# Optimization experiments

Measured on AMD Instinct MI355X. Metric: run time of the kernel, lower is better.

## Reference

```python
import jax, jax.numpy as jnp
import numpy as np

LAYERS, STACKS, K = 10, 3, 2
DILATIONS = [2 ** i for _ in range(STACKS) for i in range(LAYERS)]  # 30 layers


def conv1d(x, w, b=None, dilation=1):
    # x: [N, C_in, T], w: [C_out, C_in, K] (torch Conv1d layout), VALID padding
    out = jax.lax.conv_general_dilated(
        x, w, window_strides=(1,), padding='VALID',
        rhs_dilation=(dilation,), dimension_numbers=('NCH', 'OIH', 'NCH'))
    if b is not None:
        out = out + b[None, :, None]
    return out


def setup_inputs() -> dict:
    key = jax.random.key(0)
    ks = jax.random.split(key, 12)
    s = 0.1  # weight scale to avoid gate saturation
    return {
        'y': jax.random.normal(ks[0], (16, 1, 16384), dtype=jnp.float32),
        'causal_w': jax.random.normal(ks[1], (32, 1, 1), dtype=jnp.float32) * s,
        'causal_b': jax.random.normal(ks[2], (32,), dtype=jnp.float32) * s,
        'filt_w': jax.random.normal(ks[3], (30, 32, 32, K), dtype=jnp.float32) * s,
        'gate_w': jax.random.normal(ks[4], (30, 32, 32, K), dtype=jnp.float32) * s,
        'res_w': jax.random.normal(ks[5], (30, 32, 32, 1), dtype=jnp.float32) * s,
        'skip_w': jax.random.normal(ks[6], (30, 256, 32, 1), dtype=jnp.float32) * s,
        'end1_w': jax.random.normal(ks[7], (256, 256, 1), dtype=jnp.float32) * s,
        'end1_b': jax.random.normal(ks[8], (256,), dtype=jnp.float32) * s,
        'end2_w': jax.random.normal(ks[9], (256, 256, 1), dtype=jnp.float32) * s,
        'end2_b': jax.random.normal(ks[10], (256,), dtype=jnp.float32) * s,
    }


def reference(y, causal_w, causal_b, filt_w, gate_w, res_w, skip_w,
              end1_w, end1_b, end2_w, end2_b):
    x = conv1d(y, causal_w, causal_b)  # [B, 32, T]
    skip = None
    for i, d in enumerate(DILATIONS):
        r = x
        f = jnp.tanh(conv1d(x, filt_w[i], dilation=d))      # [B,32,T-d]
        g = jax.nn.sigmoid(conv1d(x, gate_w[i], dilation=d))
        x = f * g
        s = conv1d(x, skip_w[i])                             # [B,256,T-d]
        t = s.shape[-1]
        skip = s if skip is None else s + skip[:, :, -t:]
        x = conv1d(x, res_w[i])
        x = x + r[:, :, -x.shape[-1]:]
    x = jax.nn.relu(skip)
    x = jax.nn.relu(conv1d(x, end1_w, end1_b))
    x = conv1d(x, end2_w, end2_b)
    return x
```

## Files before the change

### kernel.cpp

```cpp
#include <hip/hip_runtime.h>
#include <hip/hip_bf16.h>
#include <cstdint>

#define NB 16
#define NC 32
#define T0 16384
#define NL 30
#define SKC 256
#define TF 13315
#define WGRP 192
#define XBC 320
#define XBS 20

typedef _Float16 f16;
typedef _Float16 f16x2 __attribute__((ext_vector_type(2)));
typedef _Float16 f16x8 __attribute__((ext_vector_type(8)));
typedef float f32x4 __attribute__((ext_vector_type(4)));
typedef uint32_t u32;

#define MFMA16(a,b,c) __builtin_amdgcn_mfma_f32_16x16x32_f16(a,b,c,0,0,0)

#define SCF (-2.88539008f)
#define SCG (-1.44269504f)
#define CLF 86.6f
#define CLG 43.3f

__device__ __forceinline__ float frcp(float x){
#if __has_builtin(__builtin_amdgcn_rcpf)
  return __builtin_amdgcn_rcpf(x);
#else
  return 1.f/x;
#endif
}
__device__ __forceinline__ float fexp2(float x){
#if __has_builtin(__builtin_amdgcn_exp2f)
  return __builtin_amdgcn_exp2f(x);
#else
  return exp2f(x);
#endif
}
__device__ __forceinline__ float clampf(float x, float c){
#if __has_builtin(__builtin_amdgcn_fmed3f)
  return __builtin_amdgcn_fmed3f(x, -c, c);
#else
  return fminf(fmaxf(x, -c), c);
#endif
}
__device__ __forceinline__ u32 pk2(float x, float y){
#if __has_builtin(__builtin_amdgcn_cvt_pkrtz)
  return __builtin_bit_cast(u32, __builtin_amdgcn_cvt_pkrtz(x, y));
#else
  f16x2 r; r.x = (f16)x; r.y = (f16)y;
  return __builtin_bit_cast(u32, r);
#endif
}
__device__ __forceinline__ u32 pkadd(u32 a, u32 b){
  f16x2 s = __builtin_bit_cast(f16x2, a) + __builtin_bit_cast(f16x2, b);
  return __builtin_bit_cast(u32, s);
}
#if __has_builtin(__builtin_amdgcn_global_load_lds)
#define HAVE_GLL 1
__device__ __forceinline__ void gll16(const void* g, void* l){
  __builtin_amdgcn_global_load_lds(
      (const __attribute__((address_space(1))) u32*)g,
      (__attribute__((address_space(3))) u32*)l, 16, 0, 0);
}
#else
#define HAVE_GLL 0
#endif
__device__ __forceinline__ size_t zfrag_off(int lz, int q){
  return (size_t)(lz & ~63)*NC + (size_t)(((lz>>4)&3)*512 + (q*16 + (lz&15))*8);
}
__device__ __forceinline__ int sigma_co(int q, int j){
  return (j < 4) ? (4*q + j) : (12 + 4*q + j);
}

__global__ __launch_bounds__(256) void prep3(
    const float* __restrict__ sw, const float* __restrict__ e1w,
    const float* __restrict__ e2w, const float* __restrict__ fw,
    const float* __restrict__ gw, const float* __restrict__ rw,
    f16* __restrict__ wsk, f16* __restrict__ e1f, f16* __restrict__ e2f,
    f16* __restrict__ fgpf, f16* __restrict__ ggpf, u32* __restrict__ rwp){
  int idx = blockIdx.x*256 + threadIdx.x;
  if (idx < 30720){
    int lane = idx & 63, mt = (idx>>6)&15, i = idx>>10;
    int m = mt*16 + (lane&15);
    int q = lane >> 4;
    const float* s = sw + ((size_t)i*SKC + m)*NC;
    f16* dp = wsk + (size_t)idx*8;
    #pragma unroll
    for (int j=0;j<8;j++) dp[j] = (f16)s[sigma_co(q, j)];
  } else if (idx < 38912){
    int j2 = idx - 30720;
    int lane = j2&63, mt = (j2>>6)&15, ks = j2>>10;
    int m = mt*16 + (lane&15);
    int k = ks*32 + (lane>>4)*8;
    const float* s = e1w + (size_t)m*SKC + k;
    f16* dp = e1f + (size_t)j2*8;
    #pragma unroll
    for (int j=0;j<8;j++) dp[j] = (f16)s[j];
  } else if (idx < 47104){
    int j2 = idx - 38912;
    int lane = j2&63, mt = (j2>>6)&15, ks = j2>>10;
    int m = mt*16 + (lane&15);
    int k = ks*32 + (lane>>4)*8;
    const float* s = e2w + (size_t)m*SKC + k;
    f16* dp = e2f + (size_t)j2*8;
    #pragma unroll
    for (int j=0;j<8;j++) dp[j] = (f16)s[j];
  } else if (idx < 77824){
    int j2 = idx - 47104;
    const float* s = fw + (size_t)j2*2;
    size_t base = (size_t)(j2 >> 5) * 64;
    int ci = j2 & 31;
    fgpf[base + ci]      = (f16)(s[0]*SCF);
    fgpf[base + 32 + ci] = (f16)(s[1]*SCF);
  } else if (idx < 108544){
    int j2 = idx - 77824;
    const float* s = gw + (size_t)j2*2;
    size_t base = (size_t)(j2 >> 5) * 64;
    int ci = j2 & 31;
    ggpf[base + ci]      = (f16)(s[0]*SCG);
    ggpf[base + 32 + ci] = (f16)(s[1]*SCG);
  } else if (idx < 123904){
    int j2 = idx - 108544;
    int i = j2 >> 9, c = (j2>>4)&31, pj = j2&15;
    const float* s = rw + ((size_t)i*NC + c)*NC;
    int q = pj >> 2, j0 = (2*pj) & 7;
    int c0 = sigma_co(q, j0);
    f16x2 p; p.x = (f16)s[c0]; p.y = (f16)s[c0+1];
    rwp[j2] = __builtin_bit_cast(u32, p);
  }
}

struct LW { f16x8 af[4]; f16x8 ag[4]; f16x8 ar[2]; };
__device__ __forceinline__ void lw_load(LW& w, const f16* __restrict__ fp,
    const f16* __restrict__ gp, const u32* __restrict__ rp, int lane){
  int m = lane & 15, q8 = (lane >> 4) * 8, q4 = (lane >> 4) * 4;
  #pragma unroll
  for (int mh = 0; mh < 2; mh++){
    #pragma unroll
    for (int tap = 0; tap < 2; tap++){
      w.af[mh*2+tap] = *(const f16x8*)&fp[((mh*16+m)*2+tap)*32 + q8];
      w.ag[mh*2+tap] = *(const f16x8*)&gp[((mh*16+m)*2+tap)*32 + q8];
    }
    w.ar[mh] = *(const f16x8*)&rp[(mh*16+m)*16 + q4];
  }
}

__device__ __forceinline__ void tile_core(const LW& w,
    uint4 a, uint4 b, uint2 rb0, uint2 rb1,
    uint4& zfrag, uint2& xo0, uint2& xo1){
  f16x8 A  = __builtin_bit_cast(f16x8, a);
  f16x8 Bt = __builtin_bit_cast(f16x8, b);
  f32x4 z4 = {0.f,0.f,0.f,0.f};
  f32x4 fa0 = MFMA16(w.af[0], A, z4); fa0 = MFMA16(w.af[1], Bt, fa0);
  f32x4 fa1 = MFMA16(w.af[2], A, z4); fa1 = MFMA16(w.af[3], Bt, fa1);
  f32x4 ga0 = MFMA16(w.ag[0], A, z4); ga0 = MFMA16(w.ag[1], Bt, ga0);
  f32x4 ga1 = MFMA16(w.ag[2], A, z4); ga1 = MFMA16(w.ag[3], Bt, ga1);
  u32 zq[4];
  #pragma unroll
  for (int mh = 0; mh < 2; mh++){
    f32x4 fv = mh ? fa1 : fa0;
    f32x4 gv = mh ? ga1 : ga0;
    float zz[4];
    #pragma unroll
    for (int r = 0; r < 4; r++){
      float t = fexp2(clampf(fv[r], CLF));
      float u = fexp2(clampf(gv[r], CLG));
      zz[r] = (1.f - t) * frcp((1.f + t) * (1.f + u));
    }
    zq[mh*2+0] = pk2(zz[0], zz[1]);
    zq[mh*2+1] = pk2(zz[2], zz[3]);
  }
  zfrag = make_uint4(zq[0], zq[1], zq[2], zq[3]);
  f16x8 zB = __builtin_bit_cast(f16x8, zfrag);
  f32x4 r0 = MFMA16(w.ar[0], zB, z4);
  f32x4 r1 = MFMA16(w.ar[1], zB, z4);
  xo0.x = pkadd(pk2(r0[0], r0[1]), rb0.x);
  xo0.y = pkadd(pk2(r0[2], r0[3]), rb0.y);
  xo1.x = pkadd(pk2(r1[0], r1[1]), rb1.x);
  xo1.y = pkadd(pk2(r1[2], r1[3]), rb1.y);
}

struct Trim7 { int t[7]; };

__global__ __launch_bounds__(256, 3) void group7m(
    const f16* __restrict__ xin, const float* __restrict__ y,
    const float* __restrict__ cw, const float* __restrict__ cb, int tc0,
    f16* __restrict__ xout, f16* __restrict__ zbase, int g0,
    int Lfinal, int TcAct, int zrows, int xpb,
    const f16* __restrict__ fgpf, const f16* __restrict__ ggpf,
    const u32* __restrict__ rwp, Trim7 trims){
  __shared__ u32 xb[2][XBC*XBS];
  int tid = threadIdx.x, b = blockIdx.y, o0 = blockIdx.x*WGRP;
  int lane = tid & 63, widx = tid >> 6;
  int Cf = Lfinal - o0; if (Cf > WGRP) Cf = WGRP;
  int Cin = Cf + 127;
  for (int p = tid; p < Cin; p += 256){
    u32* dst = &xb[0][p*XBS];
    if (y != nullptr){
      float yv = y[(size_t)b*T0 + tc0 + o0 + p];
      #pragma unroll
      for (int j = 0; j < 16; j++)
        dst[j] = pk2(fmaf(cw[2*j], yv, cb[2*j]), fmaf(cw[2*j+1], yv, cb[2*j+1]));
    } else {
      const uint4* src = (const uint4*)(xin + ((size_t)b*xpb + o0 + p)*NC);
      uint4* d4 = (uint4*)dst;
      d4[0]=src[0]; d4[1]=src[1]; d4[2]=src[2]; d4[3]=src[3];
    }
  }
  __syncthreads();
  int cur = 0;
  int tl = lane & 15, q = lane >> 4;
  size_t zlayer = (size_t)512*zrows;
  LW w;
  lw_load(w, fgpf + (size_t)g0*2048, ggpf + (size_t)g0*2048,
          rwp + (size_t)g0*512, lane);
  #pragma unroll 1
  for (int li = 0; li < 7; li++){
    int d = 1 << li;
    int count = Cf + 128 - (2 << li);
    LW wn;
    if (li < 6)
      lw_load(wn, fgpf + (size_t)(g0+li+1)*2048, ggpf + (size_t)(g0+li+1)*2048,
              rwp + (size_t)(g0+li+1)*512, lane);
    f16* zl = zbase + (size_t)(g0+li)*zlayer + (size_t)b*zrows*NC;
    int trim = trims.t[li];
    int ntiles = (count + 15) >> 4;
    for (int ti = widx; ti < ntiles; ti += 4){
      int c = ti*16 + tl;
      const u32* xc = &xb[cur][c*XBS];
      const u32* xd = &xb[cur][(c+d)*XBS];
      uint4 a  = *(const uint4*)&xc[q*4];
      uint4 b4 = *(const uint4*)&xd[q*4];
      uint2 rb0 = *(const uint2*)&xd[q*2];
      uint2 rb1 = *(const uint2*)&xd[8 + q*2];
      uint4 zf; uint2 xo0, xo1;
      tile_core(w, a, b4, rb0, rb1, zf, xo0, xo1);
      u32* xn = &xb[cur^1][c*XBS];
      *(uint2*)&xn[q*2] = xo0;
      *(uint2*)&xn[8 + q*2] = xo1;
      int lz = o0 + c - trim;
      if (c < count && lz >= 0 && lz < TcAct)
        *(uint4*)(zl + zfrag_off(lz, q)) = zf;
    }
    __syncthreads();
    if (li < 6) w = wn;
    cur ^= 1;
  }
  for (int p = tid; p < Cf; p += 256){
    const uint4* s4 = (const uint4*)&xb[cur][p*XBS];
    uint4* dd = (uint4*)(xout + ((size_t)b*xpb + o0 + p)*NC);
    dd[0]=s4[0]; dd[1]=s4[1]; dd[2]=s4[2]; dd[3]=s4[3];
  }
}

__global__ __launch_bounds__(256, 3) void singlem(
    const f16* __restrict__ xin, f16* __restrict__ xout, f16* __restrict__ zl,
    const f16* __restrict__ fp, const f16* __restrict__ gp,
    const u32* __restrict__ rp, int Tout, int d, int trim, int TcAct,
    int zrows, int xpb){
  int tid = threadIdx.x, b = blockIdx.y;
  int lane = tid & 63, widx = tid >> 6;
  int t0A = (blockIdx.x*8 + widx*2) * 16;
  if (t0A >= Tout) return;
  int haveB = (t0A + 16) < Tout;
  LW w;
  lw_load(w, fp, gp, rp, lane);
  int tl = lane & 15, q = lane >> 4;
  const f16* xbase = xin + (size_t)b*xpb*NC;
  int cA = t0A + tl;
  const f16* xcA = xbase + (size_t)cA*NC;
  const f16* xdA = xcA + (size_t)d*NC;
  uint4 aA  = *(const uint4*)(xcA + q*8);
  uint4 bA  = *(const uint4*)(xdA + q*8);
  uint2 r0A = *(const uint2*)(xdA + q*4);
  uint2 r1A = *(const uint2*)(xdA + 16 + q*4);
  int cB = cA + 16;
  const f16* xcB = xbase + (size_t)cB*NC;
  const f16* xdB = xcB + (size_t)d*NC;
  uint4 aB  = *(const uint4*)(xcB + q*8);
  uint4 bB  = *(const uint4*)(xdB + q*8);
  uint2 r0B = *(const uint2*)(xdB + q*4);
  uint2 r1B = *(const uint2*)(xdB + 16 + q*4);

  uint4 zfA, zfB; uint2 xo0A, xo1A, xo0B, xo1B;
  tile_core(w, aA, bA, r0A, r1A, zfA, xo0A, xo1A);
  tile_core(w, aB, bB, r0B, r1B, zfB, xo0B, xo1B);

  if (cA < Tout){
    f16* xoc = xout + ((size_t)b*xpb + cA)*NC;
    *(uint2*)(xoc + q*4) = xo0A;
    *(uint2*)(xoc + 16 + q*4) = xo1A;
  }
  if (haveB && cB < Tout){
    f16* xoc = xout + ((size_t)b*xpb + cB)*NC;
    *(uint2*)(xoc + q*4) = xo0B;
    *(uint2*)(xoc + 16 + q*4) = xo1B;
  }
  f16* zlb = zl + (size_t)b*zrows*NC;
  {
    int lz = cA - trim;
    if (cA < Tout && lz >= 0 && lz < TcAct)
      *(uint4*)(zlb + zfrag_off(lz, q)) = zfA;
  }
  if (haveB){
    int lz = cB - trim;
    if (cB < Tout && lz >= 0 && lz < TcAct)
      *(uint4*)(zlb + zfrag_off(lz, q)) = zfB;
  }
}

__global__ __launch_bounds__(512, 2) void skipend(
    const f16* __restrict__ zbase,
    const f16* __restrict__ wsk, const f16* __restrict__ e1f,
    const float* __restrict__ e1b, const f16* __restrict__ e2f,
    const float* __restrict__ e2b, float* __restrict__ out,
    int tc0, int TcAct, int zrows){
  __shared__ u32 smem[64*132];
  int tid = threadIdx.x, b = blockIdx.y, t0 = blockIdx.x*64;
  int w = tid>>6, lane = tid&63;
  int tl = lane & 15;
  int q  = lane >> 4;
  const uint4* wsk4 = (const uint4*)wsk;
  const uint4* e1f4 = (const uint4*)e1f;
  const uint4* e2f4 = (const uint4*)e2f;
  size_t zstepf = (size_t)512*zrows;
  const f16* zsrcb = zbase + ((size_t)b*zrows + t0)*NC;

  f32x4 acc[2][4];
  #pragma unroll
  for (int j=0;j<2;j++)
    #pragma unroll
    for (int tt=0;tt<4;tt++) acc[j][tt] = f32x4{0.f,0.f,0.f,0.f};

  auto stage = [&](int half, int lbase){
    #pragma unroll 1
    for (int s = w; s < 12; s += 8){
      int ks = s>>2, sq = s&3;
#if HAVE_GLL
      gll16(zsrcb + (size_t)(lbase+ks)*zstepf + (size_t)(sq*64+lane)*8,
            smem + (size_t)half*3072 + ks*1024 + sq*256);
#else
      uint4 v = *(const uint4*)(zsrcb + (size_t)(lbase+ks)*zstepf +
                                (size_t)(sq*64+lane)*8);
      *(uint4*)(smem + (size_t)half*3072 + ks*1024 + sq*256 + lane*4) = v;
#endif
    }
  };

  stage(0, 0);
  __syncthreads();
  #pragma unroll 1
  for (int g = 0; g < 10; g++){
    if (g < 9) stage((g+1)&1, 3*(g+1));
    const uint4* zr = (const uint4*)(smem + (size_t)(g&1)*3072);
    int lbase = g*3;
    #pragma unroll
    for (int k = 0; k < 3; k++){
      uint4 aw0 = wsk4[(size_t)(lbase+k)*1024 + (w*2+0)*64 + lane];
      uint4 aw1 = wsk4[(size_t)(lbase+k)*1024 + (w*2+1)*64 + lane];
      f16x8 zb0 = *(const f16x8*)&zr[k*256 + 0*64 + lane];
      f16x8 zb1 = *(const f16x8*)&zr[k*256 + 1*64 + lane];
      f16x8 zb2 = *(const f16x8*)&zr[k*256 + 2*64 + lane];
      f16x8 zb3 = *(const f16x8*)&zr[k*256 + 3*64 + lane];
      f16x8 a0 = __builtin_bit_cast(f16x8, aw0);
      f16x8 a1 = __builtin_bit_cast(f16x8, aw1);
      acc[0][0] = MFMA16(a0, zb0, acc[0][0]);
      acc[0][1] = MFMA16(a0, zb1, acc[0][1]);
      acc[0][2] = MFMA16(a0, zb2, acc[0][2]);
      acc[0][3] = MFMA16(a0, zb3, acc[0][3]);
      acc[1][0] = MFMA16(a1, zb0, acc[1][0]);
      acc[1][1] = MFMA16(a1, zb1, acc[1][1]);
      acc[1][2] = MFMA16(a1, zb2, acc[1][2]);
      acc[1][3] = MFMA16(a1, zb3, acc[1][3]);
    }
    __syncthreads();
  }
  int rq = q*4;
  #pragma unroll
  for (int j=0;j<2;j++){
    int c0 = (w*2+j)*16 + rq;
    #pragma unroll
    for (int tt=0;tt<4;tt++){
      int t = tt*16 + tl;
      u32 p0 = pk2(fmaxf(acc[j][tt][0],0.f), fmaxf(acc[j][tt][1],0.f));
      u32 p1 = pk2(fmaxf(acc[j][tt][2],0.f), fmaxf(acc[j][tt][3],0.f));
      *(uint2*)&smem[t*132 + (c0>>1)] = make_uint2(p0, p1);
    }
  }
  __syncthreads();
  #pragma unroll
  for (int j=0;j<2;j++)
    #pragma unroll
    for (int tt=0;tt<4;tt++) acc[j][tt] = f32x4{0.f,0.f,0.f,0.f};
  #pragma unroll
  for (int ks=0;ks<8;ks++){
    f16x8 zb[4];
    #pragma unroll
    for (int tt=0;tt<4;tt++)
      zb[tt] = *(const f16x8*)&smem[(tt*16+tl)*132 + ks*16 + q*4];
    #pragma unroll
    for (int j=0;j<2;j++){
      f16x8 a = __builtin_bit_cast(f16x8, e1f4[(size_t)(ks*16 + w*2+j)*64 + lane]);
      #pragma unroll
      for (int tt=0;tt<4;tt++)
        acc[j][tt] = MFMA16(a, zb[tt], acc[j][tt]);
    }
  }
  __syncthreads();
  #pragma unroll
  for (int j=0;j<2;j++){
    int c0 = (w*2+j)*16 + rq;
    float4 bv = *(const float4*)&e1b[c0];
    #pragma unroll
    for (int tt=0;tt<4;tt++){
      int t = tt*16 + tl;
      u32 p0 = pk2(fmaxf(acc[j][tt][0]+bv.x,0.f), fmaxf(acc[j][tt][1]+bv.y,0.f));
      u32 p1 = pk2(fmaxf(acc[j][tt][2]+bv.z,0.f), fmaxf(acc[j][tt][3]+bv.w,0.f));
      *(uint2*)&smem[t*132 + (c0>>1)] = make_uint2(p0, p1);
    }
  }
  __syncthreads();
  #pragma unroll
  for (int j=0;j<2;j++)
    #pragma unroll
    for (int tt=0;tt<4;tt++) acc[j][tt] = f32x4{0.f,0.f,0.f,0.f};
  #pragma unroll
  for (int ks=0;ks<8;ks++){
    f16x8 zb[4];
    #pragma unroll
    for (int tt=0;tt<4;tt++)
      zb[tt] = *(const f16x8*)&smem[(tt*16+tl)*132 + ks*16 + q*4];
    #pragma unroll
    for (int j=0;j<2;j++){
      f16x8 a = __builtin_bit_cast(f16x8, e2f4[(size_t)(ks*16 + w*2+j)*64 + lane]);
      #pragma unroll
      for (int tt=0;tt<4;tt++)
        acc[j][tt] = MFMA16(a, zb[tt], acc[j][tt]);
    }
  }
  #pragma unroll
  for (int j=0;j<2;j++){
    int c0 = (w*2+j)*16 + rq;
    float4 bv = *(const float4*)&e2b[c0];
    #pragma unroll
    for (int tt=0;tt<4;tt++){
      int t = tt*16 + tl;
      if (t0 + t < TcAct){
        float* op = out + ((size_t)b*SKC + c0)*TF + tc0 + t0 + t;
        op[0*TF] = acc[j][tt][0] + bv.x;
        op[1*TF] = acc[j][tt][1] + bv.y;
        op[2*TF] = acc[j][tt][2] + bv.z;
        op[3*TF] = acc[j][tt][3] + bv.w;
      }
    }
  }
}

extern "C" void kernel_launch(void* const* d_in, const int* in_sizes, int n_in,
                              void* d_out, int out_size, void* d_ws, size_t ws_size,
                              hipStream_t stream) {
  (void)in_sizes; (void)n_in; (void)out_size;
  const float* y   = (const float*)d_in[0];
  const float* cw  = (const float*)d_in[1];
  const float* cb  = (const float*)d_in[2];
  const float* fw  = (const float*)d_in[3];
  const float* gw  = (const float*)d_in[4];
  const float* rw  = (const float*)d_in[5];
  const float* sw  = (const float*)d_in[6];
  const float* e1w = (const float*)d_in[7];
  const float* e1b = (const float*)d_in[8];
  const float* e2w = (const float*)d_in[9];
  const float* e2b = (const float*)d_in[10];
  float* out = (float*)d_out;
  char* ws = (char*)d_ws;

  const size_t fixedW = 1060864;
  int TCc = 0, xpb = 0;
  for (int c = 1; c <= 6; c++){
    int tcc = (((TF + c - 1)/c) + 63) & ~63;
    int xp  = tcc + 3264;
    size_t need = fixedW + 2*(size_t)xp*1024 + (size_t)NL*512*(size_t)tcc*2;
    if (need <= ws_size){ TCc = tcc; xpb = xp; break; }
  }
  if (!TCc){ TCc = 2240; xpb = 2240 + 3264; }

  f16* wsk   = (f16*)(ws);
  f16* e1f   = (f16*)(ws +   491520);
  f16* e2f   = (f16*)(ws +   622592);
  f16* fgpf  = (f16*)(ws +  753664);
  f16* ggpf  = (f16*)(ws +  876544);
  u32* rwp   = (u32*)(ws +  999424);
  f16* xpA   = (f16*)(ws + fixedW);
  f16* xpB   = (f16*)(ws + fixedW + (size_t)xpb*1024);
  f16* zstack = (f16*)(ws + fixedW + 2*(size_t)xpb*1024);

  int S[NL+1]; S[NL] = 0;
  for (int i = NL-1; i >= 0; i--) S[i] = S[i+1] + (1 << (i % 10));

  prep3<<<dim3(484), 256, 0, stream>>>(sw, e1w, e2w, fw, gw, rw,
                                       wsk, e1f, e2f, fgpf, ggpf, rwp);

  f16* bufs[2] = {xpA, xpB};
  for (int tc0 = 0; tc0 < TF; tc0 += TCc){
    int TcAct = TF - tc0; if (TcAct > TCc) TcAct = TCc;
    int cur = 0;
    for (int s = 0; s < 3; s++){
      int g0 = s*10;
      Trim7 tr;
      for (int li = 0; li < 7; li++) tr.t[li] = S[g0+li+1];
      int Lfinal = TcAct + S[g0+7];
      const f16* gin = (s == 0) ? (const f16*)nullptr : bufs[cur];
      const float* yArg = (s == 0) ? y : (const float*)nullptr;
      int nxt = (s == 0) ? 0 : (cur ^ 1);
      group7m<<<dim3((Lfinal + WGRP-1)/WGRP, NB), 256, 0, stream>>>(
          gin, yArg, cw, cb, tc0, bufs[nxt], zstack, g0, Lfinal, TcAct,
          TCc, xpb, fgpf, ggpf, rwp, tr);
      cur = nxt;
      for (int i = g0+7; i <= g0+9; i++){
        int d = 1 << (i % 10);
        int Tout = TcAct + S[i+1];
        singlem<<<dim3((Tout + 127)/128, NB), 256, 0, stream>>>(
            bufs[cur], bufs[cur^1], zstack + (size_t)i*512*TCc,
            fgpf + (size_t)i*2048, ggpf + (size_t)i*2048, rwp + (size_t)i*512,
            Tout, d, S[i+1], TcAct, TCc, xpb);
        cur ^= 1;
      }
    }
    skipend<<<dim3((TcAct + 63)/64, NB), 512, 0, stream>>>(
        zstack, wsk, e1f, e1b, e2f, e2b, out, tc0, TcAct, TCc);
  }
}
```

Before: 657.5 us.

## Coalesce skipend output stores via LDS transpose and stage five layers per group

The skipend epilogue now writes MFMA accumulators into a per-wave LDS slab. Each lane then reads back 16 consecutive time steps and stores them as 16-byte vectors, replacing strided scalar column writes to the output. The skip accumulation loop now stages 5 layers of z per double-buffer step instead of 3, which cuts the number of barriers from 10 to 6 but enlarges shared memory. The launch-bounds occupancy hint rises from 2 to 8, which tightens the register budget and risks spills.

After: 851.3 us. +29.5%, slower.

```diff
diff --git a/kernel.cpp b/kernel.cpp
--- a/kernel.cpp
+++ b/kernel.cpp
@@ -312,13 +312,13 @@
   }
 }
 
-__global__ __launch_bounds__(512, 2) void skipend(
+__global__ __launch_bounds__(512, 8) void skipend(
     const f16* __restrict__ zbase,
     const f16* __restrict__ wsk, const f16* __restrict__ e1f,
     const float* __restrict__ e1b, const f16* __restrict__ e2f,
     const float* __restrict__ e2b, float* __restrict__ out,
     int tc0, int TcAct, int zrows){
-  __shared__ u32 smem[64*132];
+  __shared__ u32 smem[10240];
   int tid = threadIdx.x, b = blockIdx.y, t0 = blockIdx.x*64;
   int w = tid>>6, lane = tid&63;
   int tl = lane & 15;
@@ -337,15 +337,15 @@
 
   auto stage = [&](int half, int lbase){
     #pragma unroll 1
-    for (int s = w; s < 12; s += 8){
+    for (int s = w; s < 20; s += 8){
       int ks = s>>2, sq = s&3;
 #if HAVE_GLL
       gll16(zsrcb + (size_t)(lbase+ks)*zstepf + (size_t)(sq*64+lane)*8,
-            smem + (size_t)half*3072 + ks*1024 + sq*256);
+            smem + (size_t)half*5120 + ks*1024 + sq*256);
 #else
       uint4 v = *(const uint4*)(zsrcb + (size_t)(lbase+ks)*zstepf +
                                 (size_t)(sq*64+lane)*8);
-      *(uint4*)(smem + (size_t)half*3072 + ks*1024 + sq*256 + lane*4) = v;
+      *(uint4*)(smem + (size_t)half*5120 + ks*1024 + sq*256 + lane*4) = v;
 #endif
     }
   };
@@ -353,12 +353,12 @@
   stage(0, 0);
   __syncthreads();
   #pragma unroll 1
-  for (int g = 0; g < 10; g++){
-    if (g < 9) stage((g+1)&1, 3*(g+1));
-    const uint4* zr = (const uint4*)(smem + (size_t)(g&1)*3072);
-    int lbase = g*3;
-    #pragma unroll
-    for (int k = 0; k < 3; k++){
+  for (int g = 0; g < 6; g++){
+    if (g < 5) stage((g+1)&1, 5*(g+1));
+    const uint4* zr = (const uint4*)(smem + (size_t)(g&1)*5120);
+    int lbase = g*5;
+    #pragma unroll
+    for (int k = 0; k < 5; k++){
       uint4 aw0 = wsk4[(size_t)(lbase+k)*1024 + (w*2+0)*64 + lane];
       uint4 aw1 = wsk4[(size_t)(lbase+k)*1024 + (w*2+1)*64 + lane];
       f16x8 zb0 = *(const f16x8*)&zr[k*256 + 0*64 + lane];
@@ -441,6 +441,9 @@
         acc[j][tt] = MFMA16(a, zb[tt], acc[j][tt]);
     }
   }
+  __syncthreads();
+  u32* slab = smem + (size_t)w*1024;
+  int row = lane >> 2, cg = (lane & 3) * 16;
   #pragma unroll
   for (int j=0;j<2;j++){
     int c0 = (w*2+j)*16 + rq;
@@ -448,13 +451,26 @@
     #pragma unroll
     for (int tt=0;tt<4;tt++){
       int t = tt*16 + tl;
-      if (t0 + t < TcAct){
-        float* op = out + ((size_t)b*SKC + c0)*TF + tc0 + t0 + t;
-        op[0*TF] = acc[j][tt][0] + bv.x;
-        op[1*TF] = acc[j][tt][1] + bv.y;
-        op[2*TF] = acc[j][tt][2] + bv.z;
-        op[3*TF] = acc[j][tt][3] + bv.w;
-      }
+      slab[(rq+0)*64 + t] = __builtin_bit_cast(u32, acc[j][tt][0] + bv.x);
+      slab[(rq+1)*64 + t] = __builtin_bit_cast(u32, acc[j][tt][1] + bv.y);
+      slab[(rq+2)*64 + t] = __builtin_bit_cast(u32, acc[j][tt][2] + bv.z);
+      slab[(rq+3)*64 + t] = __builtin_bit_cast(u32, acc[j][tt][3] + bv.w);
+    }
+    int m0 = (w*2+j)*16;
+    const uint4* sr = (const uint4*)(slab + row*64 + cg);
+    uint4 v0 = sr[0], v1 = sr[1], v2 = sr[2], v3 = sr[3];
+    float* op = out + ((size_t)b*SKC + m0 + row)*TF + tc0 + t0 + cg;
+    if (t0 + 64 <= TcAct){
+      *(uint4*)(op)    = v0;
+      *(uint4*)(op+4)  = v1;
+      *(uint4*)(op+8)  = v2;
+      *(uint4*)(op+12) = v3;
+    } else {
+      u32 arr[16] = {v0.x,v0.y,v0.z,v0.w, v1.x,v1.y,v1.z,v1.w,
+                     v2.x,v2.y,v2.z,v2.w, v3.x,v3.y,v3.z,v3.w};
+      #pragma unroll
+      for (int e = 0; e < 16; e++)
+        if (t0 + cg + e < TcAct) op[e] = __builtin_bit_cast(float, arr[e]);
     }
   }
 }
```
